# Performance work log

Hardware: AMD Instinct MI355X
Metric: run time of the kernel (lower is better)

Reference implementation:

```python
import jax, jax.numpy as jnp
import numpy as np

B, S, D, H, Dh, F, L, V = 16, 512, 512, 8, 64, 2048, 6, 32000


def _layer_norm(x, g, b):
    m = x.mean(-1, keepdims=True)
    v = ((x - m) ** 2).mean(-1, keepdims=True)
    return (x - m) / jnp.sqrt(v + 1e-5) * g + b


def setup_inputs() -> dict:
    key = jax.random.key(0)
    ks = jax.random.split(key, 18)
    s = 0.02
    x = jax.random.randint(ks[0], (B, S), 0, V)
    batch_length = jax.random.randint(ks[1], (B,), 0, S)
    embed = (jax.random.normal(ks[2], (V, D)) * s).at[0].set(0.0)  # padding_idx=0 row zeroed
    Wq = jax.random.normal(ks[3], (L, D, H * Dh)) * s
    Wk = jax.random.normal(ks[4], (L, D, H * Dh)) * s
    Wv = jax.random.normal(ks[5], (L, D, H * Dh)) * s
    Wo = jax.random.normal(ks[6], (L, H * Dh, D)) * s
    bo = jnp.zeros((L, D))
    ln1_g = jnp.ones((L, D)); ln1_b = jnp.zeros((L, D))
    W1 = jax.random.normal(ks[7], (L, D, F)) * s
    b1 = jnp.zeros((L, F))
    W2 = jax.random.normal(ks[8], (L, F, D)) * s
    b2 = jnp.zeros((L, D))
    ln2_g = jnp.ones((L, D)); ln2_b = jnp.zeros((L, D))
    return dict(x=x, batch_length=batch_length, embed=embed, Wq=Wq, Wk=Wk, Wv=Wv,
                Wo=Wo, bo=bo, ln1_g=ln1_g, ln1_b=ln1_b, W1=W1, b1=b1, W2=W2,
                b2=b2, ln2_g=ln2_g, ln2_b=ln2_b)


def reference(x, batch_length, embed, Wq, Wk, Wv, Wo, bo, ln1_g, ln1_b,
              W1, b1, W2, b2, ln2_g, ln2_b):
    # sinusoidal positional encoding, exact replication (2.0*i/d with full index i)
    pos = jnp.arange(S, dtype=jnp.float32)[:, None]
    i = jnp.arange(D, dtype=jnp.float32)[None, :]
    ang = pos / jnp.power(10000.0, 2.0 * i / D)
    pe = ang.at[:, 0::2].set(jnp.sin(ang[:, 0::2])).at[:, 1::2].set(jnp.cos(ang[:, 1::2]))
    # per-sample PE truncated at batch_length (rest zero)
    len_mask = (jnp.arange(S)[None, :] < batch_length[:, None]).astype(pe.dtype)
    h = embed[x] + pe[None, :, :] * len_mask[:, :, None]  # [B,S,D]
    # padding mask: True where token==0, expanded to [B,S,S]; torch repeat(H,1,1) -> heads major
    pad = (x == 0)
    pmask = jnp.broadcast_to(pad[:, None, :], (B, S, S))
    mrep = jnp.tile(pmask, (H, 1, 1))  # [H*B, S, S], faithful to torch .repeat
    scale = 1.0 / np.sqrt(Dh).astype(np.float32)
    for l in range(L):
        # faithful .view(B*H, -1, Dh) on [B,S,H*Dh] contiguous memory
        q = (h @ Wq[l]).reshape(B * H, S, Dh)
        k = (h @ Wk[l]).reshape(B * H, S, Dh)
        v = (h @ Wv[l]).reshape(B * H, S, Dh)
        att = jnp.einsum('bqd,bkd->bqk', q, k) * scale  # [B*H,S,S]
        att = jnp.where(mrep, -1e9, att)
        att = jax.nn.softmax(att, axis=2)
        ctx = (att @ v).reshape(B, S, H * Dh)
        o = ctx @ Wo[l] + bo[l]
        h = _layer_norm(h + o, ln1_g[l], ln1_b[l])
        f = jax.nn.relu(h @ W1[l] + b1[l]) @ W2[l] + b2[l]
        h = _layer_norm(h + f, ln2_g[l], ln2_b[l])
    return h
```

## Files before the change

### kernel.cpp

```cpp
#include <hip/hip_runtime.h>
#include <hip/hip_bf16.h>
#include <cmath>

#define B_  16
#define S_  512
#define D_  512
#define F_  2048
#define L_  6
#define MT  8192

typedef __attribute__((ext_vector_type(8))) __bf16 bf16x8;
typedef __attribute__((ext_vector_type(4))) float  f32x4;

__device__ __forceinline__ unsigned short f2bf(float f) {
  return __builtin_bit_cast(unsigned short, __float2bfloat16(f));
}

__device__ __forceinline__ void gload16(const void* g, void* l) {
  __builtin_amdgcn_global_load_lds(
      (const __attribute__((address_space(1))) void*)g,
      (__attribute__((address_space(3))) void*)l, 16, 0, 0);
}

__global__ void embed_pe_kernel(const int* __restrict__ x,
                                const int* __restrict__ blen,
                                const float* __restrict__ emb,
                                float* __restrict__ h,
                                unsigned short* __restrict__ hbf) {
  int bs = blockIdx.x;
  int b = bs >> 9, s = bs & 511;
  int tok = x[bs];
  bool pe = s < blen[b];
  const float* er = emb + (long)tok * D_;
  long rb = (long)bs * D_;
  for (int d = threadIdx.x; d < D_; d += 256) {
    float e = er[d];
    if (pe) {
      float ex = (2.0f * (float)d) / 512.0f;
      float ang = (float)s / powf(10000.0f, ex);
      e += (d & 1) ? cosf(ang) : sinf(ang);
    }
    h[rb + d] = e;
    hbf[rb + d] = f2bf(e);
  }
}

__global__ void mask_build_kernel(const int* __restrict__ x,
                                  unsigned int* __restrict__ mw) {
  int t = threadIdx.x;
  int b = t >> 4, wd = t & 15;
  unsigned int m = 0;
  for (int j = 0; j < 32; j++)
    if (x[b * 512 + wd * 32 + j] == 0) m |= (1u << j);
  mw[b * 16 + wd] = m;
}

__global__ __launch_bounds__(256)
void wconv_kernel(const float* __restrict__ in, unsigned short* __restrict__ out,
                  int K, int N, long inls, long outls) {
  __shared__ float tile[32][33];
  const float* ip = in + (long)blockIdx.z * inls;
  unsigned short* op = out + (long)blockIdx.z * outls;
  int k0 = blockIdx.y * 32, n0 = blockIdx.x * 32;
  int tx = threadIdx.x & 31, ty = threadIdx.x >> 5;
  for (int i = ty; i < 32; i += 8) tile[i][tx] = ip[(long)(k0 + i) * N + n0 + tx];
  __syncthreads();
  for (int i = ty; i < 32; i += 8) op[(long)(n0 + i) * K + k0 + tx] = f2bf(tile[tx][i]);
}

template<int BMv, int MINW>
__global__ __launch_bounds__(256, MINW)
void gemm_bf16(const unsigned short* __restrict__ A,
               const unsigned short* __restrict__ Bt,
               const float* __restrict__ bias,
               float* __restrict__ C, unsigned short* __restrict__ Cbf,
               int M, int N, int K, int relu, int qkv) {
  constexpr int MFR = 4;
  constexpr int NFR = (BMv == 128) ? 4 : 2;
  __shared__ unsigned short Al[2][BMv * 32];
  __shared__ unsigned short Bl[2][128 * 32];
  int t = threadIdx.x;
  int lane = t & 63, wid = t >> 6;

  int flat = blockIdx.y * gridDim.x + blockIdx.x;
  int npx = (gridDim.x * gridDim.y) >> 3;
  int w = (flat & 7) * npx + (flat >> 3);
  int bx = w % gridDim.x, by = w / gridDim.x;

  int rbase = by * BMv, cbase = bx * 128;
  int wr = (BMv == 128) ? (wid >> 1) * 64 : 0;
  int wc = (BMv == 128) ? (wid & 1) * 64 : wid * 32;

  f32x4 acc[MFR][NFR];
#pragma unroll
  for (int i = 0; i < MFR; i++)
#pragma unroll
    for (int j = 0; j < NFR; j++) acc[i][j] = (f32x4){0.f, 0.f, 0.f, 0.f};

  int srow = t >> 2;
  int sc = (((t & 3) ^ ((t >> 3) & 3)) << 3);
  const unsigned short* Ag  = A  + (long)(rbase + srow) * K + sc;
  const unsigned short* Ag2 = A  + (long)(rbase + 64 + srow) * K + sc;
  const unsigned short* Bg  = Bt + (long)(cbase + srow) * K + sc;
  const unsigned short* Bg2 = Bt + (long)(cbase + 64 + srow) * K + sc;

  auto stage = [&](int bi, int kt) {
    gload16(Ag + kt, &Al[bi][t * 8]);
    if constexpr (BMv == 128) gload16(Ag2 + kt, &Al[bi][2048 + t * 8]);
    gload16(Bg + kt, &Bl[bi][t * 8]);
    gload16(Bg2 + kt, &Bl[bi][2048 + t * 8]);
  };

  int fr = lane & 15;
  int c4 = lane >> 4;

  int nt = K >> 5;
  stage(0, 0);
  int cur = 0;
  for (int tt = 0; tt < nt; ++tt) {
    if (tt + 1 < nt) {
      stage(cur ^ 1, (tt + 1) << 5);
      if constexpr (BMv == 128)
        asm volatile("s_waitcnt vmcnt(4)" ::: "memory");
      else
        asm volatile("s_waitcnt vmcnt(3)" ::: "memory");
    } else {
      asm volatile("s_waitcnt vmcnt(0)" ::: "memory");
    }
    __builtin_amdgcn_s_barrier();

    bf16x8 a[MFR], b[NFR];
#pragma unroll
    for (int m = 0; m < MFR; m++) {
      int R = wr + m * 16 + fr;
      a[m] = *(const bf16x8*)&Al[cur][R * 32 + ((c4 ^ ((R >> 1) & 3)) << 3)];
    }
#pragma unroll
    for (int n = 0; n < NFR; n++) {
      int R = wc + n * 16 + fr;
      b[n] = *(const bf16x8*)&Bl[cur][R * 32 + ((c4 ^ ((R >> 1) & 3)) << 3)];
    }
#pragma unroll
    for (int m = 0; m < MFR; m++)
#pragma unroll
      for (int n = 0; n < NFR; n++)
        acc[m][n] = __builtin_amdgcn_mfma_f32_16x16x32_bf16(a[m], b[n], acc[m][n], 0, 0, 0);
    __builtin_amdgcn_s_barrier();
    cur ^= 1;
  }

  if (BMv == 128 && qkv) {
#pragma unroll
    for (int m = 0; m < MFR; m++) {
#pragma unroll
      for (int n = 0; n < NFR; n++) {
        int col = cbase + wc + n * 16 + fr;
#pragma unroll
        for (int j = 0; j < 4; j++) {
          long row = rbase + wr + m * 16 + (lane >> 4) * 4 + j;
          unsigned short v = f2bf(acc[m][n][j]);
          if (col < 1024) {
            Cbf[(col < 512 ? 0L : 4194304L - 512L) + row * 512 + col] = v;
          } else {
            int cc = col - 1024;
            Cbf[8388608L + (row >> 6) * 32768 + (long)(cc & 63) * 512 +
                ((row & 63) << 3) + (cc >> 6)] = v;
          }
        }
      }
    }
  } else {
#pragma unroll
    for (int m = 0; m < MFR; m++) {
#pragma unroll
      for (int n = 0; n < NFR; n++) {
        int col = cbase + wc + n * 16 + fr;
        float bv = bias ? bias[col] : 0.0f;
#pragma unroll
        for (int j = 0; j < 4; j++) {
          long row = rbase + wr + m * 16 + (lane >> 4) * 4 + j;
          float v = acc[m][n][j] + bv;
          if (relu) v = fmaxf(v, 0.0f);
          if (C)   C[row * N + col] = v;
          if (Cbf) Cbf[row * N + col] = f2bf(v);
        }
      }
    }
  }
}

__global__ __launch_bounds__(512, 4)
void attn_mfma(const unsigned short* __restrict__ qbf,
               const unsigned short* __restrict__ kbf,
               const unsigned short* __restrict__ vtbf,
               const unsigned int* __restrict__ maskw,
               unsigned short* __restrict__ ctxbf) {
  __shared__ unsigned short sb[4][8192];
  __shared__ float red[2][8][64];
  int t = threadIdx.x;
  int lane = t & 63, w = t >> 6;
  int qg = w & 3, kh = w >> 2;
  int c = lane & 15, h = lane >> 4;

  int flat = blockIdx.y * 8 + blockIdx.x;
  int wk = (flat & 7) * 128 + (flat >> 3);
  int qt = wk & 7, bh = wk >> 3;

  long bhb = (long)bh << 15;
  int mb = bh & 15;

  unsigned int mwa[16];
#pragma unroll
  for (int i = 0; i < 16; i++)
    mwa[i] = (unsigned int)__builtin_amdgcn_readfirstlane((int)maskw[mb * 16 + i]);

  const bf16x8* qp = (const bf16x8*)(qbf + bhb + (long)(qt * 64 + qg * 16 + c) * 64);
  bf16x8 qf0 = qp[h], qf1 = qp[h + 4];

  auto stageK = [&](int gc) {
#pragma unroll
    for (int i = 0; i < 2; i++) {
      int idx = t + 512 * i;
      int kr = idx >> 3, g = idx & 7;
      gload16(kbf + bhb + (long)(gc * 128 + kr) * 64 + ((g ^ (kr & 7)) << 3),
              &sb[gc][idx * 8]);
    }
  };
  auto stageV = [&](int gc) {
#pragma unroll
    for (int i = 0; i < 2; i++) {
      int idx = t + 512 * i;
      int d = idx >> 4, g = idx & 15;
      gload16(vtbf + bhb + (long)d * 512 + gc * 128 + ((g ^ (d & 15)) << 3),
              &sb[gc][idx * 8]);
    }
  };

  stageK(0); stageK(2); stageK(1); stageK(3);

  f32x4 acc[16];
#pragma unroll
  for (int F = 0; F < 16; F++) acc[F] = (f32x4){0.f, 0.f, 0.f, 0.f};

#pragma unroll
  for (int lc = 0; lc < 2; lc++) {
    if (lc == 0) asm volatile("s_waitcnt vmcnt(4)" ::: "memory");
    else         asm volatile("s_waitcnt vmcnt(0)" ::: "memory");
    __builtin_amdgcn_s_barrier();
    const unsigned short* kb = sb[kh * 2 + lc];
#pragma unroll
    for (int f = 0; f < 8; f++) {
      int R = f * 16 + c;
      int ro = R * 64;
      bf16x8 a0 = *(const bf16x8*)&kb[ro + ((h ^ (R & 7)) << 3)];
      bf16x8 a1 = *(const bf16x8*)&kb[ro + (((h + 4) ^ (R & 7)) << 3)];
      acc[lc * 8 + f] = __builtin_amdgcn_mfma_f32_16x16x32_bf16(a0, qf0, acc[lc * 8 + f], 0, 0, 0);
      acc[lc * 8 + f] = __builtin_amdgcn_mfma_f32_16x16x32_bf16(a1, qf1, acc[lc * 8 + f], 0, 0, 0);
    }
  }
  __builtin_amdgcn_s_barrier();

  stageV(0); stageV(2); stageV(1); stageV(3);

#pragma unroll
  for (int F = 0; F < 16; F++) {
    int gc = kh * 2 + (F >> 3), f = F & 7;
    unsigned int nib = (mwa[gc * 4 + (f >> 1)] >> (((f & 1) << 4) + (h << 2))) & 0xFu;
#pragma unroll
    for (int j = 0; j < 4; j++)
      acc[F][j] = (nib & (1u << j)) ? -1e9f : acc[F][j] * 0.125f;
  }

  float mx = -3.0e38f;
#pragma unroll
  for (int F = 0; F < 16; F++)
#pragma unroll
    for (int j = 0; j < 4; j++) mx = fmaxf(mx, acc[F][j]);
  mx = fmaxf(mx, __shfl_xor(mx, 16));
  mx = fmaxf(mx, __shfl_xor(mx, 32));
  red[0][w][lane] = mx;
  __builtin_amdgcn_s_barrier();
  mx = fmaxf(mx, red[0][w ^ 4][lane]);

  float sm = 0.f;
  unsigned int pk[32];
#pragma unroll
  for (int F = 0; F < 16; F++) {
    float e0 = __expf(acc[F][0] - mx); sm += e0;
    float e1 = __expf(acc[F][1] - mx); sm += e1;
    float e2 = __expf(acc[F][2] - mx); sm += e2;
    float e3 = __expf(acc[F][3] - mx); sm += e3;
    pk[2 * F]     = (unsigned int)f2bf(e0) | ((unsigned int)f2bf(e1) << 16);
    pk[2 * F + 1] = (unsigned int)f2bf(e2) | ((unsigned int)f2bf(e3) << 16);
  }
  sm += __shfl_xor(sm, 16);
  sm += __shfl_xor(sm, 32);
  red[1][w][lane] = sm;
  __builtin_amdgcn_s_barrier();
  sm += red[1][w ^ 4][lane];

  float rs0 = 1.0f / __shfl(sm, h * 4 + 0);
  float rs1 = 1.0f / __shfl(sm, h * 4 + 1);
  float rs2 = 1.0f / __shfl(sm, h * 4 + 2);
  float rs3 = 1.0f / __shfl(sm, h * 4 + 3);

  f32x4 o[4];
#pragma unroll
  for (int n = 0; n < 4; n++) o[n] = (f32x4){0.f, 0.f, 0.f, 0.f};
  int l0 = c | ((lane & 16) << 1);
  int l1 = l0 + 16;
  bool hb = (lane & 32) != 0;

#pragma unroll
  for (int lc = 0; lc < 2; lc++) {
    if (lc == 0) asm volatile("s_waitcnt vmcnt(4)" ::: "memory");
    else         asm volatile("s_waitcnt vmcnt(0)" ::: "memory");
    __builtin_amdgcn_s_barrier();
    const unsigned short* vbuf = sb[kh * 2 + lc];
#pragma unroll
    for (int sub = 0; sub < 4; sub++) {
      int kt4 = (lc * 4 + sub) * 4;
      unsigned int a0 = __shfl((int)pk[kt4],     l0);
      unsigned int a1 = __shfl((int)pk[kt4 + 1], l0);
      unsigned int a2 = __shfl((int)pk[kt4],     l1);
      unsigned int a3 = __shfl((int)pk[kt4 + 1], l1);
      unsigned int b0 = __shfl((int)pk[kt4 + 2], l0);
      unsigned int b1 = __shfl((int)pk[kt4 + 3], l0);
      unsigned int b2 = __shfl((int)pk[kt4 + 2], l1);
      unsigned int b3 = __shfl((int)pk[kt4 + 3], l1);
      uint4 aw;
      aw.x = hb ? b0 : a0; aw.y = hb ? b1 : a1;
      aw.z = hb ? b2 : a2; aw.w = hb ? b3 : a3;
      bf16x8 af = __builtin_bit_cast(bf16x8, aw);
#pragma unroll
      for (int n = 0; n < 4; n++) {
        int dl = n * 16 + c;
        bf16x8 vf = *(const bf16x8*)&vbuf[dl * 128 + (((sub * 4 + h) ^ (dl & 15)) << 3)];
        o[n] = __builtin_amdgcn_mfma_f32_16x16x32_bf16(af, vf, o[n], 0, 0, 0);
      }
    }
  }
  __builtin_amdgcn_s_barrier();

  float* osb = (float*)sb;
  if (kh) {
#pragma unroll
    for (int n = 0; n < 4; n++)
#pragma unroll
      for (int j = 0; j < 4; j++)
        osb[((w - 4) * 64 + lane) * 16 + n * 4 + j] = o[n][j];
  }
  __builtin_amdgcn_s_barrier();
  if (!kh) {
    unsigned short* cp = ctxbf + bhb + (long)(qt * 64 + qg * 16) * 64;
#pragma unroll
    for (int n = 0; n < 4; n++) {
      float t0 = o[n][0] + osb[(w * 64 + lane) * 16 + n * 4 + 0];
      float t1 = o[n][1] + osb[(w * 64 + lane) * 16 + n * 4 + 1];
      float t2 = o[n][2] + osb[(w * 64 + lane) * 16 + n * 4 + 2];
      float t3 = o[n][3] + osb[(w * 64 + lane) * 16 + n * 4 + 3];
      cp[(h * 4 + 0) * 64 + n * 16 + c] = f2bf(t0 * rs0);
      cp[(h * 4 + 1) * 64 + n * 16 + c] = f2bf(t1 * rs1);
      cp[(h * 4 + 2) * 64 + n * 16 + c] = f2bf(t2 * rs2);
      cp[(h * 4 + 3) * 64 + n * 16 + c] = f2bf(t3 * rs3);
    }
  }
}

__global__ __launch_bounds__(256)
void ln_kernel(const float* __restrict__ a, const float* __restrict__ r,
               const float* __restrict__ g, const float* __restrict__ be,
               float* __restrict__ out, unsigned short* __restrict__ outbf) {
  int w = threadIdx.x >> 6, lane = threadIdx.x & 63;
  long row = (long)blockIdx.x * 4 + w;
  long base = row * D_ + lane * 8;
  float4 a0 = *(const float4*)(a + base);
  float4 a1 = *(const float4*)(a + base + 4);
  float4 r0 = *(const float4*)(r + base);
  float4 r1 = *(const float4*)(r + base + 4);
  float xv[8] = {a0.x + r0.x, a0.y + r0.y, a0.z + r0.z, a0.w + r0.w,
                 a1.x + r1.x, a1.y + r1.y, a1.z + r1.z, a1.w + r1.w};
  float s = 0;
#pragma unroll
  for (int e = 0; e < 8; e++) s += xv[e];
#pragma unroll
  for (int off = 1; off < 64; off <<= 1) s += __shfl_xor(s, off);
  float m = s * (1.0f / 512.0f);
  float vs = 0;
#pragma unroll
  for (int e = 0; e < 8; e++) { float d = xv[e] - m; vs += d * d; }
#pragma unroll
  for (int off = 1; off < 64; off <<= 1) vs += __shfl_xor(vs, off);
  float rstd = 1.0f / sqrtf(vs * (1.0f / 512.0f) + 1e-5f);
  int gb = lane * 8;
  float o[8];
#pragma unroll
  for (int e = 0; e < 8; e++) o[e] = (xv[e] - m) * rstd * g[gb + e] + be[gb + e];
  *(float4*)(out + base)     = make_float4(o[0], o[1], o[2], o[3]);
  *(float4*)(out + base + 4) = make_float4(o[4], o[5], o[6], o[7]);
  ushort4 u0, u1;
  u0.x = f2bf(o[0]); u0.y = f2bf(o[1]); u0.z = f2bf(o[2]); u0.w = f2bf(o[3]);
  u1.x = f2bf(o[4]); u1.y = f2bf(o[5]); u1.z = f2bf(o[6]); u1.w = f2bf(o[7]);
  *(ushort4*)(outbf + base)     = u0;
  *(ushort4*)(outbf + base + 4) = u1;
}

extern "C" void kernel_launch(void* const* d_in, const int* in_sizes, int n_in,
                              void* d_out, int out_size, void* d_ws, size_t ws_size,
                              hipStream_t stream) {
  const int*   x    = (const int*)d_in[0];
  const int*   blen = (const int*)d_in[1];
  const float* emb  = (const float*)d_in[2];
  const float* Wq   = (const float*)d_in[3];
  const float* Wk   = (const float*)d_in[4];
  const float* Wv   = (const float*)d_in[5];
  const float* Wo   = (const float*)d_in[6];
  const float* bo   = (const float*)d_in[7];
  const float* ln1g = (const float*)d_in[8];
  const float* ln1b = (const float*)d_in[9];
  const float* W1   = (const float*)d_in[10];
  const float* b1   = (const float*)d_in[11];
  const float* W2   = (const float*)d_in[12];
  const float* b2   = (const float*)d_in[13];
  const float* ln2g = (const float*)d_in[14];
  const float* ln2b = (const float*)d_in[15];
  float* out = (float*)d_out;

  float* ws_f = (float*)d_ws;
  const long M4 = 4194304L;
  float* h   = ws_f;
  float* tmp = ws_f + M4;
  unsigned short* U = (unsigned short*)(ws_f + 2 * M4);
  unsigned short* h_bf   = U;
  unsigned short* q_bf   = U + M4;
  unsigned short* k_bf   = U + 2 * M4;
  unsigned short* vt_bf  = U + 3 * M4;
  unsigned short* ctx_bf = U + 4 * M4;
  unsigned short* mid_bf = q_bf;
  unsigned short* Wqkvt  = U + 5 * M4;
  unsigned short* Wot    = Wqkvt + 6L * 1536 * 512;
  unsigned short* W1t    = Wot   + 6L * 512 * 512;
  unsigned short* W2t    = W1t   + 6L * 2048 * 512;
  unsigned int*   maskw  = (unsigned int*)(W2t + 6L * 512 * 2048);

  wconv_kernel<<<dim3(16, 16, 6), 256, 0, stream>>>(Wq, Wqkvt,            512, 512,  262144L, 786432L);
  wconv_kernel<<<dim3(16, 16, 6), 256, 0, stream>>>(Wk, Wqkvt + 262144,   512, 512,  262144L, 786432L);
  wconv_kernel<<<dim3(16, 16, 6), 256, 0, stream>>>(Wv, Wqkvt + 524288,   512, 512,  262144L, 786432L);
  wconv_kernel<<<dim3(16, 16, 6), 256, 0, stream>>>(Wo, Wot,              512, 512,  262144L, 262144L);
  wconv_kernel<<<dim3(64, 16, 6), 256, 0, stream>>>(W1, W1t,              512, 2048, 1048576L, 1048576L);
  wconv_kernel<<<dim3(16, 64, 6), 256, 0, stream>>>(W2, W2t,              2048, 512, 1048576L, 1048576L);
  mask_build_kernel<<<1, 256, 0, stream>>>(x, maskw);
  embed_pe_kernel<<<MT, 256, 0, stream>>>(x, blen, emb, h, h_bf);

  dim3 gqkv(12, 64), g2048(16, 64), g512b(4, 128), gattn(8, 128);

  for (int l = 0; l < L_; l++) {
    const unsigned short* wqkv = Wqkvt + (long)l * 1536 * 512;
    const unsigned short* wo   = Wot   + (long)l * 512 * 512;
    const unsigned short* w1   = W1t   + (long)l * 2048 * 512;
    const unsigned short* w2   = W2t   + (long)l * 512 * 2048;

    gemm_bf16<128, 2><<<gqkv, 256, 0, stream>>>(h_bf, wqkv, nullptr, nullptr, q_bf,
                                                MT, 1536, 512, 0, 1);
    attn_mfma<<<gattn, 512, 0, stream>>>(q_bf, k_bf, vt_bf, maskw, ctx_bf);
    gemm_bf16<64, 3><<<g512b, 256, 0, stream>>>(ctx_bf, wo, bo + (long)l * D_, tmp, nullptr,
                                                MT, 512, 512, 0, 0);
    ln_kernel<<<MT / 4, 256, 0, stream>>>(h, tmp, ln1g + (long)l * D_,
                                          ln1b + (long)l * D_, h, h_bf);
    gemm_bf16<128, 2><<<g2048, 256, 0, stream>>>(h_bf, w1, b1 + (long)l * F_, nullptr, mid_bf,
                                                 MT, 2048, 512, 1, 0);
    gemm_bf16<64, 3><<<g512b, 256, 0, stream>>>(mid_bf, w2, b2 + (long)l * D_, tmp, nullptr,
                                                MT, 512, 2048, 0, 0);
    ln_kernel<<<MT / 4, 256, 0, stream>>>(h, tmp, ln2g + (long)l * D_,
                                          ln2b + (long)l * D_,
                                          (l == L_ - 1) ? out : h, h_bf);
  }
}
```

Before: 1.019 ms.

## Stage GEMM epilogue through LDS for vector stores; move V transpose to separate kernel

The GEMM epilogue now writes accumulators into a per-wave padded LDS buffer and re-reads them so each lane emits 16-byte vectorized global stores, for both the bf16 and fp32 outputs. This replaces the scattered 2-byte and 4-byte stores of the old epilogue. The QKV epilogue now writes V in plain row layout, and a new vtrans_kernel transposes it per head through shared memory into a buffer aliased on tmp. The cost is an extra kernel launch and a full read and write of V each layer, plus an extra barrier and LDS round trip in every GEMM.

```diff
diff --git a/kernel.cpp b/kernel.cpp
--- a/kernel.cpp
+++ b/kernel.cpp
@@ -68,6 +68,29 @@
   for (int i = ty; i < 32; i += 8) op[(long)(n0 + i) * K + k0 + tx] = f2bf(tile[tx][i]);
 }
 
+__global__ __launch_bounds__(256)
+void vtrans_kernel(const unsigned short* __restrict__ v,
+                   unsigned short* __restrict__ vt) {
+  __shared__ unsigned short tl[64][72];
+  int bh = blockIdx.x;
+  const unsigned short* ip = v + (long)bh * 32768;
+  unsigned short* op = vt + (long)bh * 32768;
+  int t = threadIdx.x;
+  int kv = t >> 2, g = t & 3;
+  int dh = t >> 2, q4 = t & 3;
+  for (int c0 = 0; c0 < 512; c0 += 64) {
+    __syncthreads();
+    *(uint4*)&tl[kv][g * 16]     = *(const uint4*)&ip[(long)(c0 + kv) * 64 + g * 16];
+    *(uint4*)&tl[kv][g * 16 + 8] = *(const uint4*)&ip[(long)(c0 + kv) * 64 + g * 16 + 8];
+    __syncthreads();
+    unsigned short tmp[16];
+#pragma unroll
+    for (int e = 0; e < 16; e++) tmp[e] = tl[q4 * 16 + e][dh];
+    *(uint4*)&op[(long)dh * 512 + c0 + q4 * 16]     = *(uint4*)&tmp[0];
+    *(uint4*)&op[(long)dh * 512 + c0 + q4 * 16 + 8] = *(uint4*)&tmp[8];
+  }
+}
+
 template<int BMv, int MINW>
 __global__ __launch_bounds__(256, MINW)
 void gemm_bf16(const unsigned short* __restrict__ A,
@@ -77,8 +100,9 @@
                int M, int N, int K, int relu, int qkv) {
   constexpr int MFR = 4;
   constexpr int NFR = (BMv == 128) ? 4 : 2;
-  __shared__ unsigned short Al[2][BMv * 32];
-  __shared__ unsigned short Bl[2][128 * 32];
+  __shared__ float smemf[8448];
+  unsigned short* Al = (unsigned short*)smemf;
+  unsigned short* Bl = Al + 2 * BMv * 32;
   int t = threadIdx.x;
   int lane = t & 63, wid = t >> 6;
 
@@ -105,10 +129,10 @@
   const unsigned short* Bg2 = Bt + (long)(cbase + 64 + srow) * K + sc;
 
   auto stage = [&](int bi, int kt) {
-    gload16(Ag + kt, &Al[bi][t * 8]);
-    if constexpr (BMv == 128) gload16(Ag2 + kt, &Al[bi][2048 + t * 8]);
-    gload16(Bg + kt, &Bl[bi][t * 8]);
-    gload16(Bg2 + kt, &Bl[bi][2048 + t * 8]);
+    gload16(Ag + kt, Al + bi * BMv * 32 + t * 8);
+    if constexpr (BMv == 128) gload16(Ag2 + kt, Al + bi * BMv * 32 + 2048 + t * 8);
+    gload16(Bg + kt, Bl + bi * 4096 + t * 8);
+    gload16(Bg2 + kt, Bl + bi * 4096 + 2048 + t * 8);
   };
 
   int fr = lane & 15;
@@ -133,12 +157,12 @@
 #pragma unroll
     for (int m = 0; m < MFR; m++) {
       int R = wr + m * 16 + fr;
-      a[m] = *(const bf16x8*)&Al[cur][R * 32 + ((c4 ^ ((R >> 1) & 3)) << 3)];
+      a[m] = *(const bf16x8*)&Al[cur * BMv * 32 + R * 32 + ((c4 ^ ((R >> 1) & 3)) << 3)];
     }
 #pragma unroll
     for (int n = 0; n < NFR; n++) {
       int R = wc + n * 16 + fr;
-      b[n] = *(const bf16x8*)&Bl[cur][R * 32 + ((c4 ^ ((R >> 1) & 3)) << 3)];
+      b[n] = *(const bf16x8*)&Bl[cur * 4096 + R * 32 + ((c4 ^ ((R >> 1) & 3)) << 3)];
     }
 #pragma unroll
     for (int m = 0; m < MFR; m++)
@@ -149,41 +173,56 @@
     cur ^= 1;
   }
 
-  if (BMv == 128 && qkv) {
-#pragma unroll
-    for (int m = 0; m < MFR; m++) {
-#pragma unroll
-      for (int n = 0; n < NFR; n++) {
-        int col = cbase + wc + n * 16 + fr;
+  __syncthreads();
+  float* wb = smemf + wid * 2112;
+  int cb0 = cbase + wc;
+#pragma unroll
+  for (int nh = 0; nh < NFR / 2; nh++) {
+#pragma unroll
+    for (int mi = 0; mi < MFR; mi++)
+#pragma unroll
+      for (int n2 = 0; n2 < 2; n2++) {
+        int n = nh * 2 + n2;
+        int col = cb0 + nh * 32 + n2 * 16 + fr;
+        float bv = bias ? bias[col] : 0.0f;
 #pragma unroll
         for (int j = 0; j < 4; j++) {
-          long row = rbase + wr + m * 16 + (lane >> 4) * 4 + j;
-          unsigned short v = f2bf(acc[m][n][j]);
-          if (col < 1024) {
-            Cbf[(col < 512 ? 0L : 4194304L - 512L) + row * 512 + col] = v;
-          } else {
-            int cc = col - 1024;
-            Cbf[8388608L + (row >> 6) * 32768 + (long)(cc & 63) * 512 +
-                ((row & 63) << 3) + (cc >> 6)] = v;
-          }
+          float v = acc[mi][n][j] + bv;
+          if (relu) v = fmaxf(v, 0.0f);
+          wb[(mi * 16 + (lane >> 4) * 4 + j) * 33 + n2 * 16 + fr] = v;
         }
       }
-    }
-  } else {
-#pragma unroll
-    for (int m = 0; m < MFR; m++) {
-#pragma unroll
-      for (int n = 0; n < NFR; n++) {
-        int col = cbase + wc + n * 16 + fr;
-        float bv = bias ? bias[col] : 0.0f;
-#pragma unroll
-        for (int j = 0; j < 4; j++) {
-          long row = rbase + wr + m * 16 + (lane >> 4) * 4 + j;
-          float v = acc[m][n][j] + bv;
-          if (relu) v = fmaxf(v, 0.0f);
-          if (C)   C[row * N + col] = v;
-          if (Cbf) Cbf[row * N + col] = f2bf(v);
+    if (Cbf) {
+      int rl0 = lane >> 2, g = lane & 3;
+#pragma unroll
+      for (int i = 0; i < 4; i++) {
+        int rl = i * 16 + rl0;
+        long grow = rbase + wr + rl;
+        int gcol = cb0 + nh * 32 + g * 8;
+        unsigned short tmp[8];
+#pragma unroll
+        for (int e = 0; e < 8; e++) tmp[e] = f2bf(wb[rl * 33 + g * 8 + e]);
+        unsigned short* dst;
+        if (qkv) {
+          long off = (gcol < 512) ? 0L
+                     : (gcol < 1024 ? 4194304L - 512L : 8388608L - 1024L);
+          dst = Cbf + off + grow * 512 + gcol;
+        } else {
+          dst = Cbf + grow * (long)N + gcol;
         }
+        *(uint4*)dst = *(uint4*)tmp;
+      }
+    }
+    if (C) {
+      int rl0 = lane >> 3, g = lane & 7;
+#pragma unroll
+      for (int i = 0; i < 8; i++) {
+        int rl = i * 8 + rl0;
+        long grow = rbase + wr + rl;
+        int gcol = cb0 + nh * 32 + g * 4;
+        float4 vv = make_float4(wb[rl * 33 + g * 4],     wb[rl * 33 + g * 4 + 1],
+                                wb[rl * 33 + g * 4 + 2], wb[rl * 33 + g * 4 + 3]);
+        *(float4*)(C + grow * (long)N + gcol) = vv;
       }
     }
   }
@@ -434,8 +473,9 @@
   unsigned short* h_bf   = U;
   unsigned short* q_bf   = U + M4;
   unsigned short* k_bf   = U + 2 * M4;
-  unsigned short* vt_bf  = U + 3 * M4;
+  unsigned short* v_bf   = U + 3 * M4;
   unsigned short* ctx_bf = U + 4 * M4;
+  unsigned short* vt_bf  = (unsigned short*)tmp;
   unsigned short* mid_bf = q_bf;
   unsigned short* Wqkvt  = U + 5 * M4;
   unsigned short* Wot    = Wqkvt + 6L * 1536 * 512;
@@ -462,6 +502,7 @@
 
     gemm_bf16<128, 2><<<gqkv, 256, 0, stream>>>(h_bf, wqkv, nullptr, nullptr, q_bf,
                                                 MT, 1536, 512, 0, 1);
+    vtrans_kernel<<<128, 256, 0, stream>>>(v_bf, vt_bf);
     attn_mfma<<<gattn, 512, 0, stream>>>(q_bf, k_bf, vt_bf, maskw, ctx_bf);
     gemm_bf16<64, 3><<<g512b, 256, 0, stream>>>(ctx_bf, wo, bo + (long)l * D_, tmp, nullptr,
                                                 MT, 512, 512, 0, 0);
```

Measured after the change: 922.4 us. 1.1x faster.
